# Performance work log

Hardware: AMD Instinct MI355X
Metric: run time of the kernel (lower is better)

The kernel has to match this reference:

```python
import jax, jax.numpy as jnp
import numpy as np

B, NFIELD, NEMB, NFILTER, NLAYERS = 256, 64, 64, 128, 3


def setup_inputs() -> dict:
    key = jax.random.key(0)
    ks = jax.random.split(key, 5)
    x = jax.random.normal(ks[0], (B, NFIELD, NEMB), dtype=jnp.float32)
    # Conv1d(k=1, bias=False) weights, squeezed to (out_ch, in_ch). Small init for stability.
    W0 = jax.random.normal(ks[1], (NFILTER, NFIELD * NFIELD), dtype=jnp.float32) * 0.02
    W1 = jax.random.normal(ks[2], (NFILTER, NFIELD * NFILTER), dtype=jnp.float32) * 0.02
    W2 = jax.random.normal(ks[3], (NFILTER, NFIELD * NFILTER), dtype=jnp.float32) * 0.02
    Wa = jax.random.normal(ks[4], (1, NLAYERS * NFILTER), dtype=jnp.float32) * 0.02
    return {"x": x, "W0": W0, "W1": W1, "W2": W2, "Wa": Wa}


def reference(x, W0, W1, W2, Wa):
    # x: (B, F, E). CIN recurrence over a fixed small number of layers.
    Ws = [W0, W1, W2]
    x0 = x
    xk = x
    pooled = []
    for W in Ws:
        # outer product over field axes: (B, F, C, E)
        h = x0[:, :, None, :] * xk[:, None, :, :]
        b, f, c, e = h.shape
        h = h.reshape(b, f * c, e)
        # 1x1 conv == GEMM over channel dim, then ReLU
        xk = jax.nn.relu(jnp.einsum('oc,bce->boe', W, h))
        # sum-pool over embedding dim: (B, nfilter)
        pooled.append(jnp.sum(xk, axis=-1))
    feats = jnp.concatenate(pooled, axis=1)  # (B, nlayers*nfilter)
    y = feats @ Wa.T                         # (B, 1)
    return y[:, 0]
```

## Files before the change

### kernel.cpp

```cpp
#include <hip/hip_runtime.h>

#define NBATCH 256
#define NFILT  128

typedef __attribute__((ext_vector_type(8))) short bf16x8;
typedef __attribute__((ext_vector_type(4))) float f32x4;

__device__ __forceinline__ unsigned short f2b(float f) {
    unsigned u = __float_as_uint(f);
    u = (u + 0x7fffu + ((u >> 16) & 1u)) >> 16;
    return (unsigned short)u;
}
__device__ __forceinline__ float b2f(unsigned short h) {
    return __uint_as_float(((unsigned)h) << 16);
}
__device__ __forceinline__ void async16(const void* g, void* l) {
    __builtin_amdgcn_global_load_lds((const __attribute__((address_space(1))) unsigned int*)g,
                                     (__attribute__((address_space(3))) unsigned int*)l, 16, 0, 0);
}

#define XKA_OFF 0
#define XKB_OFF 16384
#define X0T_OFF 32768
#define X0F_OFF 40960
#define RED_OFF 49152
#define YS_OFF  147456
#define SMEM_SZ 147520

__global__ void prep_all(const float* __restrict__ x,
                         const float* __restrict__ W0,
                         const float* __restrict__ W1,
                         const float* __restrict__ W2,
                         unsigned short* __restrict__ x0t,
                         unsigned short* __restrict__ x0f,
                         unsigned short* __restrict__ Wp0,
                         unsigned short* __restrict__ Wp1,
                         unsigned short* __restrict__ Wp2)
{
    const int bid = blockIdx.x, tid = threadIdx.x;
    if (bid < 10240) {
        const float* W; unsigned short* Wp; int CLOG, KLOG, idx;
        if (bid < 2048)      { W = W0; Wp = Wp0; CLOG = 6; KLOG = 12; idx = bid * 256 + tid; }
        else if (bid < 6144) { W = W1; Wp = Wp1; CLOG = 7; KLOG = 13; idx = (bid - 2048) * 256 + tid; }
        else                 { W = W2; Wp = Wp2; CLOG = 7; KLOG = 13; idx = (bid - 6144) * 256 + tid; }
        int o = idx >> KLOG, k = idx & ((1 << KLOG) - 1);
        int f = k >> CLOG, c = k & ((1 << CLOG) - 1);
        int kg = f >> 4, fl = f & 15;
        int cs = c >> 5, kseg = (c >> 3) & 3, j = c & 7;
        int mh = o >> 6, mt = (o >> 4) & 3, l15 = o & 15;
        int ncs = 1 << (CLOG - 5);
        size_t dst = ((((size_t)((kg * 16 + fl) * ncs + cs) * 2 + mh) * 4 + mt) * 64
                      + kseg * 16 + l15) * 8 + j;
        Wp[dst] = f2b(W[idx]);
    } else {
        int idx = (bid - 10240) * 256 + tid;
        int b = idx >> 12, r = idx & 4095, f = r >> 6, e = r & 63;
        unsigned short v = f2b(x[idx]);
        x0f[b * 4096 + f * 64 + e] = v;
        x0t[b * 4096 + e * 64 + ((((f >> 3) ^ (e & 7)) << 3) | (f & 7))] = v;
    }
}

template<int NCS, int ROWB, bool LAST>
__device__ __forceinline__ void do_layer(
    const char* __restrict__ Ag,
    const char* __restrict__ XKsrc,
    char* __restrict__ XKdst,
    const char* __restrict__ X0F,
    char* __restrict__ RED,
    const float* __restrict__ Wa_l,
    float& ypart, int lane, int l15, int kseg, int e7, int mh, int kg)
{
    const f32x4 ZERO = {0.f, 0.f, 0.f, 0.f};
    f32x4 acc[4][4];
#pragma unroll
    for (int mt = 0; mt < 4; ++mt)
#pragma unroll
        for (int nt = 0; nt < 4; ++nt) acc[mt][nt] = ZERO;

    bf16x8 bq[NCS][4];
#pragma unroll
    for (int cs = 0; cs < NCS; ++cs)
#pragma unroll
        for (int nt = 0; nt < 4; ++nt)
            bq[cs][nt] = *(const bf16x8*)(XKsrc + (nt * 16 + l15) * ROWB
                                          + ((((cs << 2) + kseg) ^ e7) << 4));

    bf16x8 aq[2][4];
#pragma unroll
    for (int mt = 0; mt < 4; ++mt)
        aq[0][mt] = *(const bf16x8*)(Ag + mt * 1024);

    f32x4 accf[4][4];
    for (int fl = 0; fl < 16; ++fl) {
        const unsigned short* xf = (const unsigned short*)(X0F + ((kg * 16 + fl) << 7));
        const float x0v0 = b2f(xf[l15]);
        const float x0v1 = b2f(xf[16 + l15]);
        const float x0v2 = b2f(xf[32 + l15]);
        const float x0v3 = b2f(xf[48 + l15]);
        const size_t ksf = (size_t)fl * NCS;
#pragma unroll
        for (int cs = 0; cs < NCS; ++cs) {
#pragma unroll
            for (int mt = 0; mt < 4; ++mt)
                aq[(cs + 1) & 1][mt] =
                    *(const bf16x8*)(Ag + (ksf + cs + 1) * 8192 + mt * 1024);
#pragma unroll
            for (int mt = 0; mt < 4; ++mt)
#pragma unroll
                for (int nt = 0; nt < 4; ++nt)
                    accf[mt][nt] = __builtin_amdgcn_mfma_f32_16x16x32_bf16(
                        aq[cs & 1][mt], bq[cs][nt],
                        (cs == 0) ? ZERO : accf[mt][nt], 0, 0, 0);
        }
#pragma unroll
        for (int mt = 0; mt < 4; ++mt) {
            acc[mt][0] += accf[mt][0] * x0v0;
            acc[mt][1] += accf[mt][1] * x0v1;
            acc[mt][2] += accf[mt][2] * x0v2;
            acc[mt][3] += accf[mt][3] * x0v3;
        }
    }

    if (kg != 0) {
        char* slot = RED + (mh * 3 + (kg - 1)) * 16384;
#pragma unroll
        for (int mt = 0; mt < 4; ++mt)
#pragma unroll
            for (int nt = 0; nt < 4; ++nt)
                *(f32x4*)(slot + ((mt * 4 + nt) * 64 + lane) * 16) = acc[mt][nt];
    }
    __syncthreads();
    if (kg == 0) {
#pragma unroll
        for (int s = 0; s < 3; ++s) {
            const char* slot = RED + (mh * 3 + s) * 16384;
#pragma unroll
            for (int mt = 0; mt < 4; ++mt)
#pragma unroll
                for (int nt = 0; nt < 4; ++nt)
                    acc[mt][nt] += *(const f32x4*)(slot + ((mt * 4 + nt) * 64 + lane) * 16);
        }
        const int r0 = (lane >> 4) * 4;
#pragma unroll
        for (int mt = 0; mt < 4; ++mt) {
            const int om = mh * 64 + mt * 16 + r0;
            const float4 wa = *(const float4*)(Wa_l + om);
            const int osw = (((om >> 3) ^ e7) << 4) | ((om & 7) << 1);
#pragma unroll
            for (int nt = 0; nt < 4; ++nt) {
                f32x4 v = acc[mt][nt];
                v.x = fmaxf(v.x, 0.f); v.y = fmaxf(v.y, 0.f);
                v.z = fmaxf(v.z, 0.f); v.w = fmaxf(v.w, 0.f);
                ypart = fmaf(wa.x, v.x, ypart);
                ypart = fmaf(wa.y, v.y, ypart);
                ypart = fmaf(wa.z, v.z, ypart);
                ypart = fmaf(wa.w, v.w, ypart);
                if (!LAST) {
                    unsigned lo = (unsigned)f2b(v.x) | ((unsigned)f2b(v.y) << 16);
                    unsigned hi = (unsigned)f2b(v.z) | ((unsigned)f2b(v.w) << 16);
                    *(uint2*)(XKdst + (nt * 16 + l15) * 256 + osw) = make_uint2(lo, hi);
                }
            }
        }
    }
    __syncthreads();
}

__global__ __launch_bounds__(512, 2) void cin_main(
    const unsigned short* __restrict__ Wp0,
    const unsigned short* __restrict__ Wp1,
    const unsigned short* __restrict__ Wp2,
    const unsigned short* __restrict__ x0t,
    const unsigned short* __restrict__ x0f,
    const float* __restrict__ Wa,
    float* __restrict__ y)
{
    extern __shared__ char sm[];
    const int b = blockIdx.x, tid = threadIdx.x;
    const int lane = tid & 63, w = tid >> 6;
    const int mh = w & 1, kg = w >> 1;
    const int l15 = lane & 15, kseg = lane >> 4, e7 = lane & 7;

    async16((const char*)x0t + (size_t)b * 8192 + w * 1024 + lane * 16,
            sm + X0T_OFF + w * 1024);
    async16((const char*)x0f + (size_t)b * 8192 + w * 1024 + lane * 16,
            sm + X0F_OFF + w * 1024);
    __syncthreads();

    float ypart = 0.f;
    const char* Ag0 = (const char*)Wp0 + (size_t)kg * 16 * 2 * 8192 + mh * 4096 + lane * 16;
    do_layer<2, 128, false>(Ag0, sm + X0T_OFF, sm + XKA_OFF, sm + X0F_OFF, sm + RED_OFF,
                            Wa + 0, ypart, lane, l15, kseg, e7, mh, kg);
    const char* Ag1 = (const char*)Wp1 + (size_t)kg * 16 * 4 * 8192 + mh * 4096 + lane * 16;
    do_layer<4, 256, false>(Ag1, sm + XKA_OFF, sm + XKB_OFF, sm + X0F_OFF, sm + RED_OFF,
                            Wa + 128, ypart, lane, l15, kseg, e7, mh, kg);
    const char* Ag2 = (const char*)Wp2 + (size_t)kg * 16 * 4 * 8192 + mh * 4096 + lane * 16;
    do_layer<4, 256, true>(Ag2, sm + XKB_OFF, sm + XKA_OFF, sm + X0F_OFF, sm + RED_OFF,
                           Wa + 256, ypart, lane, l15, kseg, e7, mh, kg);

#pragma unroll
    for (int off = 32; off >= 1; off >>= 1)
        ypart += __shfl_down(ypart, off, 64);
    float* YS = (float*)(sm + YS_OFF);
    if (lane == 0 && kg == 0) YS[mh] = ypart;
    __syncthreads();
    if (tid == 0) y[b] = YS[0] + YS[1];
}

extern "C" void kernel_launch(void* const* d_in, const int* in_sizes, int n_in,
                              void* d_out, int out_size, void* d_ws, size_t ws_size,
                              hipStream_t stream) {
    const float* x  = (const float*)d_in[0];
    const float* W0 = (const float*)d_in[1];
    const float* W1 = (const float*)d_in[2];
    const float* W2 = (const float*)d_in[3];
    const float* Wa = (const float*)d_in[4];
    float* y = (float*)d_out;

    char* ws = (char*)d_ws;
    unsigned short* Wp0 = (unsigned short*)(ws);
    unsigned short* Wp1 = (unsigned short*)(ws + (1u << 20));
    unsigned short* Wp2 = (unsigned short*)(ws + (3u << 20));
    unsigned short* x0t = (unsigned short*)(ws + (5u << 20));
    unsigned short* x0f = (unsigned short*)(ws + (7u << 20));

    hipLaunchKernelGGL(prep_all, dim3(14336), dim3(256), 0, stream,
                       x, W0, W1, W2, x0t, x0f, Wp0, Wp1, Wp2);

    hipFuncSetAttribute((const void*)cin_main, hipFuncAttributeMaxDynamicSharedMemorySize, SMEM_SZ);
    hipLaunchKernelGGL(cin_main, dim3(NBATCH), dim3(512), SMEM_SZ, stream,
                       Wp0, Wp1, Wp2, x0t, x0f, Wa, y);
}
```

Measured before the change: 102.2 us.

## Split fused CIN kernel into per-layer kernels tiled by batch and output row group

Replaces the single per-batch kernel, where each block ran all three layers with a cross-wave K-split reduction through LDS, with one kernel launch per layer plus a small finalize kernel. Each block now handles 8 batches (one per wave) and a 16-row output group, so no LDS reduction or intra-block barriers are needed. The weight layout is repacked by row group so each wave streams a contiguous A slice, and intermediate xk goes through global memory. This adds kernel launches and global round-trips of activations, and each wave fetches the same weight slice separately.

New measurement: 118.9 us. 1.16x slower.

```diff
diff --git a/kernel.cpp b/kernel.cpp
--- a/kernel.cpp
+++ b/kernel.cpp
@@ -18,14 +18,6 @@
     __builtin_amdgcn_global_load_lds((const __attribute__((address_space(1))) unsigned int*)g,
                                      (__attribute__((address_space(3))) unsigned int*)l, 16, 0, 0);
 }
-
-#define XKA_OFF 0
-#define XKB_OFF 16384
-#define X0T_OFF 32768
-#define X0F_OFF 40960
-#define RED_OFF 49152
-#define YS_OFF  147456
-#define SMEM_SZ 147520
 
 __global__ void prep_all(const float* __restrict__ x,
                          const float* __restrict__ W0,
@@ -45,167 +37,149 @@
         else                 { W = W2; Wp = Wp2; CLOG = 7; KLOG = 13; idx = (bid - 6144) * 256 + tid; }
         int o = idx >> KLOG, k = idx & ((1 << KLOG) - 1);
         int f = k >> CLOG, c = k & ((1 << CLOG) - 1);
-        int kg = f >> 4, fl = f & 15;
+        int rg = o >> 4, l15 = o & 15;
         int cs = c >> 5, kseg = (c >> 3) & 3, j = c & 7;
-        int mh = o >> 6, mt = (o >> 4) & 3, l15 = o & 15;
-        int ncs = 1 << (CLOG - 5);
-        size_t dst = ((((size_t)((kg * 16 + fl) * ncs + cs) * 2 + mh) * 4 + mt) * 64
-                      + kseg * 16 + l15) * 8 + j;
+        int NCS = 1 << (CLOG - 5);
+        int NK = 64 * NCS;
+        int kstep = f * NCS + cs;
+        size_t dst = (((size_t)rg * NK + kstep) * 64 + kseg * 16 + l15) * 8 + j;
         Wp[dst] = f2b(W[idx]);
     } else {
         int idx = (bid - 10240) * 256 + tid;
         int b = idx >> 12, r = idx & 4095, f = r >> 6, e = r & 63;
         unsigned short v = f2b(x[idx]);
         x0f[b * 4096 + f * 64 + e] = v;
-        x0t[b * 4096 + e * 64 + ((((f >> 3) ^ (e & 7)) << 3) | (f & 7))] = v;
-    }
-}
-
-template<int NCS, int ROWB, bool LAST>
-__device__ __forceinline__ void do_layer(
-    const char* __restrict__ Ag,
-    const char* __restrict__ XKsrc,
-    char* __restrict__ XKdst,
-    const char* __restrict__ X0F,
-    char* __restrict__ RED,
+        x0t[b * 4096 + e * 64 + f] = v;
+    }
+}
+
+template <int CL, bool LAST>
+__global__ __launch_bounds__(512) void layer_k(
+    const unsigned short* __restrict__ Wp,
+    const unsigned short* __restrict__ Bsrc,
+    const unsigned short* __restrict__ x0f,
     const float* __restrict__ Wa_l,
-    float& ypart, int lane, int l15, int kseg, int e7, int mh, int kg)
+    unsigned short* __restrict__ xknext,
+    float* __restrict__ ybuf)
 {
+    constexpr int NCS = CL / 32;
+    constexpr int NK  = 64 * NCS;
+    constexpr int NG  = NK / 4;
+    extern __shared__ char sm[];
+    const int bid = blockIdx.x, tid = threadIdx.x;
+    const int rg = bid & 7, sg = bid >> 3;
+    const int lane = tid & 63, w = tid >> 6;
+    const int l15 = lane & 15, kseg = lane >> 4;
+    const int b = sg * 8 + w;
+
+    {
+        const char* src = (const char*)x0f + (size_t)b * 8192 + lane * 16;
+        char* dst = sm + w * 8192;
+#pragma unroll
+        for (int i = 0; i < 8; ++i) async16(src + i * 1024, dst + i * 1024);
+    }
+
+    bf16x8 bq[NCS][4];
+    const char* Bb = (const char*)Bsrc + (size_t)b * (CL * 128) + kseg * 16;
+#pragma unroll
+    for (int cs = 0; cs < NCS; ++cs)
+#pragma unroll
+        for (int nt = 0; nt < 4; ++nt)
+            bq[cs][nt] = *(const bf16x8*)(Bb + (nt * 16 + l15) * (CL * 2) + cs * 64);
+
+    const char* Ag = (const char*)Wp + ((size_t)rg * NK) * 1024 + (kseg * 16 + l15) * 16;
+    bf16x8 aq[4];
+    aq[0] = *(const bf16x8*)(Ag);
+    aq[1] = *(const bf16x8*)(Ag + 1024);
+
+    __syncthreads();
+
+    const unsigned short* XF = (const unsigned short*)(sm + w * 8192);
     const f32x4 ZERO = {0.f, 0.f, 0.f, 0.f};
-    f32x4 acc[4][4];
-#pragma unroll
-    for (int mt = 0; mt < 4; ++mt)
-#pragma unroll
-        for (int nt = 0; nt < 4; ++nt) acc[mt][nt] = ZERO;
-
-    bf16x8 bq[NCS][4];
-#pragma unroll
-    for (int cs = 0; cs < NCS; ++cs)
-#pragma unroll
-        for (int nt = 0; nt < 4; ++nt)
-            bq[cs][nt] = *(const bf16x8*)(XKsrc + (nt * 16 + l15) * ROWB
-                                          + ((((cs << 2) + kseg) ^ e7) << 4));
-
-    bf16x8 aq[2][4];
-#pragma unroll
-    for (int mt = 0; mt < 4; ++mt)
-        aq[0][mt] = *(const bf16x8*)(Ag + mt * 1024);
-
-    f32x4 accf[4][4];
-    for (int fl = 0; fl < 16; ++fl) {
-        const unsigned short* xf = (const unsigned short*)(X0F + ((kg * 16 + fl) << 7));
-        const float x0v0 = b2f(xf[l15]);
-        const float x0v1 = b2f(xf[16 + l15]);
-        const float x0v2 = b2f(xf[32 + l15]);
-        const float x0v3 = b2f(xf[48 + l15]);
-        const size_t ksf = (size_t)fl * NCS;
-#pragma unroll
-        for (int cs = 0; cs < NCS; ++cs) {
-#pragma unroll
-            for (int mt = 0; mt < 4; ++mt)
-                aq[(cs + 1) & 1][mt] =
-                    *(const bf16x8*)(Ag + (ksf + cs + 1) * 8192 + mt * 1024);
-#pragma unroll
-            for (int mt = 0; mt < 4; ++mt)
-#pragma unroll
-                for (int nt = 0; nt < 4; ++nt)
-                    accf[mt][nt] = __builtin_amdgcn_mfma_f32_16x16x32_bf16(
-                        aq[cs & 1][mt], bq[cs][nt],
-                        (cs == 0) ? ZERO : accf[mt][nt], 0, 0, 0);
-        }
-#pragma unroll
-        for (int mt = 0; mt < 4; ++mt) {
-            acc[mt][0] += accf[mt][0] * x0v0;
-            acc[mt][1] += accf[mt][1] * x0v1;
-            acc[mt][2] += accf[mt][2] * x0v2;
-            acc[mt][3] += accf[mt][3] * x0v3;
-        }
-    }
-
-    if (kg != 0) {
-        char* slot = RED + (mh * 3 + (kg - 1)) * 16384;
-#pragma unroll
-        for (int mt = 0; mt < 4; ++mt)
-#pragma unroll
-            for (int nt = 0; nt < 4; ++nt)
-                *(f32x4*)(slot + ((mt * 4 + nt) * 64 + lane) * 16) = acc[mt][nt];
-    }
-    __syncthreads();
-    if (kg == 0) {
-#pragma unroll
-        for (int s = 0; s < 3; ++s) {
-            const char* slot = RED + (mh * 3 + s) * 16384;
-#pragma unroll
-            for (int mt = 0; mt < 4; ++mt)
-#pragma unroll
-                for (int nt = 0; nt < 4; ++nt)
-                    acc[mt][nt] += *(const f32x4*)(slot + ((mt * 4 + nt) * 64 + lane) * 16);
-        }
-        const int r0 = (lane >> 4) * 4;
-#pragma unroll
-        for (int mt = 0; mt < 4; ++mt) {
-            const int om = mh * 64 + mt * 16 + r0;
-            const float4 wa = *(const float4*)(Wa_l + om);
-            const int osw = (((om >> 3) ^ e7) << 4) | ((om & 7) << 1);
+    f32x4 acc[4], accf[4];
+#pragma unroll
+    for (int nt = 0; nt < 4; ++nt) acc[nt] = ZERO;
+
+    for (int g = 0; g < NG; ++g) {
+        const size_t k0 = (size_t)g * 4;
+        float sA[4], sB[4];
+        if (NCS == 4) {
+#pragma unroll
+            for (int nt = 0; nt < 4; ++nt) sA[nt] = b2f(XF[g * 64 + nt * 16 + l15]);
+        } else {
 #pragma unroll
             for (int nt = 0; nt < 4; ++nt) {
-                f32x4 v = acc[mt][nt];
-                v.x = fmaxf(v.x, 0.f); v.y = fmaxf(v.y, 0.f);
-                v.z = fmaxf(v.z, 0.f); v.w = fmaxf(v.w, 0.f);
-                ypart = fmaf(wa.x, v.x, ypart);
-                ypart = fmaf(wa.y, v.y, ypart);
-                ypart = fmaf(wa.z, v.z, ypart);
-                ypart = fmaf(wa.w, v.w, ypart);
-                if (!LAST) {
-                    unsigned lo = (unsigned)f2b(v.x) | ((unsigned)f2b(v.y) << 16);
-                    unsigned hi = (unsigned)f2b(v.z) | ((unsigned)f2b(v.w) << 16);
-                    *(uint2*)(XKdst + (nt * 16 + l15) * 256 + osw) = make_uint2(lo, hi);
-                }
+                sA[nt] = b2f(XF[(2 * g) * 64 + nt * 16 + l15]);
+                sB[nt] = b2f(XF[(2 * g + 1) * 64 + nt * 16 + l15]);
             }
         }
-    }
-    __syncthreads();
-}
-
-__global__ __launch_bounds__(512, 2) void cin_main(
-    const unsigned short* __restrict__ Wp0,
-    const unsigned short* __restrict__ Wp1,
-    const unsigned short* __restrict__ Wp2,
-    const unsigned short* __restrict__ x0t,
-    const unsigned short* __restrict__ x0f,
-    const float* __restrict__ Wa,
-    float* __restrict__ y)
-{
-    extern __shared__ char sm[];
-    const int b = blockIdx.x, tid = threadIdx.x;
-    const int lane = tid & 63, w = tid >> 6;
-    const int mh = w & 1, kg = w >> 1;
-    const int l15 = lane & 15, kseg = lane >> 4, e7 = lane & 7;
-
-    async16((const char*)x0t + (size_t)b * 8192 + w * 1024 + lane * 16,
-            sm + X0T_OFF + w * 1024);
-    async16((const char*)x0f + (size_t)b * 8192 + w * 1024 + lane * 16,
-            sm + X0F_OFF + w * 1024);
-    __syncthreads();
-
+        aq[2] = *(const bf16x8*)(Ag + (k0 + 2) * 1024);
+#pragma unroll
+        for (int nt = 0; nt < 4; ++nt)
+            accf[nt] = __builtin_amdgcn_mfma_f32_16x16x32_bf16(aq[0], bq[0][nt], ZERO, 0, 0, 0);
+        aq[3] = *(const bf16x8*)(Ag + (k0 + 3) * 1024);
+#pragma unroll
+        for (int nt = 0; nt < 4; ++nt)
+            accf[nt] = __builtin_amdgcn_mfma_f32_16x16x32_bf16(aq[1], bq[1 & (NCS - 1)][nt], accf[nt], 0, 0, 0);
+        if (NCS == 2) {
+#pragma unroll
+            for (int nt = 0; nt < 4; ++nt) {
+                const f32x4 sv = {sA[nt], sA[nt], sA[nt], sA[nt]};
+                acc[nt] += accf[nt] * sv;
+            }
+        }
+        aq[0] = *(const bf16x8*)(Ag + (k0 + 4) * 1024);
+#pragma unroll
+        for (int nt = 0; nt < 4; ++nt)
+            accf[nt] = __builtin_amdgcn_mfma_f32_16x16x32_bf16(aq[2], bq[2 & (NCS - 1)][nt],
+                                                               (NCS == 2) ? ZERO : accf[nt], 0, 0, 0);
+        aq[1] = *(const bf16x8*)(Ag + (k0 + 5) * 1024);
+#pragma unroll
+        for (int nt = 0; nt < 4; ++nt)
+            accf[nt] = __builtin_amdgcn_mfma_f32_16x16x32_bf16(aq[3], bq[3 & (NCS - 1)][nt], accf[nt], 0, 0, 0);
+        {
+            const float* sf = (NCS == 2) ? sB : sA;
+#pragma unroll
+            for (int nt = 0; nt < 4; ++nt) {
+                const f32x4 sv = {sf[nt], sf[nt], sf[nt], sf[nt]};
+                acc[nt] += accf[nt] * sv;
+            }
+        }
+    }
+
+    const float4 wa = *(const float4*)(Wa_l + rg * 16 + kseg * 4);
     float ypart = 0.f;
-    const char* Ag0 = (const char*)Wp0 + (size_t)kg * 16 * 2 * 8192 + mh * 4096 + lane * 16;
-    do_layer<2, 128, false>(Ag0, sm + X0T_OFF, sm + XKA_OFF, sm + X0F_OFF, sm + RED_OFF,
-                            Wa + 0, ypart, lane, l15, kseg, e7, mh, kg);
-    const char* Ag1 = (const char*)Wp1 + (size_t)kg * 16 * 4 * 8192 + mh * 4096 + lane * 16;
-    do_layer<4, 256, false>(Ag1, sm + XKA_OFF, sm + XKB_OFF, sm + X0F_OFF, sm + RED_OFF,
-                            Wa + 128, ypart, lane, l15, kseg, e7, mh, kg);
-    const char* Ag2 = (const char*)Wp2 + (size_t)kg * 16 * 4 * 8192 + mh * 4096 + lane * 16;
-    do_layer<4, 256, true>(Ag2, sm + XKB_OFF, sm + XKA_OFF, sm + X0F_OFF, sm + RED_OFF,
-                           Wa + 256, ypart, lane, l15, kseg, e7, mh, kg);
-
+#pragma unroll
+    for (int nt = 0; nt < 4; ++nt) {
+        f32x4 v = acc[nt];
+        v.x = fmaxf(v.x, 0.f); v.y = fmaxf(v.y, 0.f);
+        v.z = fmaxf(v.z, 0.f); v.w = fmaxf(v.w, 0.f);
+        ypart = fmaf(wa.x, v.x, ypart);
+        ypart = fmaf(wa.y, v.y, ypart);
+        ypart = fmaf(wa.z, v.z, ypart);
+        ypart = fmaf(wa.w, v.w, ypart);
+        if (!LAST) {
+            unsigned lo = (unsigned)f2b(v.x) | ((unsigned)f2b(v.y) << 16);
+            unsigned hi = (unsigned)f2b(v.z) | ((unsigned)f2b(v.w) << 16);
+            *(uint2*)((char*)xknext + (size_t)b * 16384 + (nt * 16 + l15) * 256
+                      + (rg * 16 + kseg * 4) * 2) = make_uint2(lo, hi);
+        }
+    }
 #pragma unroll
     for (int off = 32; off >= 1; off >>= 1)
         ypart += __shfl_down(ypart, off, 64);
-    float* YS = (float*)(sm + YS_OFF);
-    if (lane == 0 && kg == 0) YS[mh] = ypart;
-    __syncthreads();
-    if (tid == 0) y[b] = YS[0] + YS[1];
+    if (lane == 0) ybuf[b * 8 + rg] = ypart;
+}
+
+__global__ void finalize_k(const float* __restrict__ ybuf, float* __restrict__ y) {
+    const int b = threadIdx.x;
+    float s = 0.f;
+#pragma unroll
+    for (int l = 0; l < 3; ++l)
+#pragma unroll
+        for (int r = 0; r < 8; ++r)
+            s += ybuf[l * 2048 + b * 8 + r];
+    y[b] = s;
 }
 
 extern "C" void kernel_launch(void* const* d_in, const int* in_sizes, int n_in,
@@ -219,16 +193,31 @@
     float* y = (float*)d_out;
 
     char* ws = (char*)d_ws;
-    unsigned short* Wp0 = (unsigned short*)(ws);
-    unsigned short* Wp1 = (unsigned short*)(ws + (1u << 20));
-    unsigned short* Wp2 = (unsigned short*)(ws + (3u << 20));
-    unsigned short* x0t = (unsigned short*)(ws + (5u << 20));
-    unsigned short* x0f = (unsigned short*)(ws + (7u << 20));
+    unsigned short* Wp0  = (unsigned short*)(ws + 0x000000);
+    unsigned short* Wp1  = (unsigned short*)(ws + 0x110000);
+    unsigned short* Wp2  = (unsigned short*)(ws + 0x320000);
+    unsigned short* x0t  = (unsigned short*)(ws + 0x530000);
+    unsigned short* x0f  = (unsigned short*)(ws + 0x730000);
+    unsigned short* xkA  = (unsigned short*)(ws + 0x930000);
+    unsigned short* xkB  = (unsigned short*)(ws + 0xD30000);
+    float*          ybuf = (float*)(ws + 0x1130000);
 
     hipLaunchKernelGGL(prep_all, dim3(14336), dim3(256), 0, stream,
                        x, W0, W1, W2, x0t, x0f, Wp0, Wp1, Wp2);
 
-    hipFuncSetAttribute((const void*)cin_main, hipFuncAttributeMaxDynamicSharedMemorySize, SMEM_SZ);
-    hipLaunchKernelGGL(cin_main, dim3(NBATCH), dim3(512), SMEM_SZ, stream,
-                       Wp0, Wp1, Wp2, x0t, x0f, Wa, y);
-}
+    hipFuncSetAttribute((const void*)layer_k<64, false>,
+                        hipFuncAttributeMaxDynamicSharedMemorySize, 65536);
+    hipFuncSetAttribute((const void*)layer_k<128, false>,
+                        hipFuncAttributeMaxDynamicSharedMemorySize, 65536);
+    hipFuncSetAttribute((const void*)layer_k<128, true>,
+                        hipFuncAttributeMaxDynamicSharedMemorySize, 65536);
+
+    hipLaunchKernelGGL((layer_k<64, false>), dim3(256), dim3(512), 65536, stream,
+                       Wp0, x0t, x0f, Wa + 0, xkA, ybuf + 0);
+    hipLaunchKernelGGL((layer_k<128, false>), dim3(256), dim3(512), 65536, stream,
+                       Wp1, xkA, x0f, Wa + 128, xkB, ybuf + 2048);
+    hipLaunchKernelGGL((layer_k<128, true>), dim3(256), dim3(512), 65536, stream,
+                       Wp2, xkB, x0f, Wa + 256, xkA, ybuf + 4096);
+
+    hipLaunchKernelGGL(finalize_k, dim3(1), dim3(256), 0, stream, ybuf, y);
+}
```
